# Performance work log

Measured on AMD Instinct MI355X. Metric: run time of the kernel, lower is better.

Reference implementation:

```python
import jax, jax.numpy as jnp
import numpy as np

D_STATE = 128   # Mamba2 default (the SS2D d_state=16 is never forwarded to Mamba2)
N_HEADS = 4     # d_ssm // headdim = d_model / (d_model//4)
D_CONV = 4
EPS = 1e-5


def silu(v):
    return v * jax.nn.sigmoid(v)


def setup_inputs() -> dict:
    key = jax.random.key(0)
    ks = jax.random.split(key, 12)
    d_model = 256
    d_inner = 2 * d_model            # expand=2
    d_ssm = d_model
    conv_dim = d_ssm + 2 * D_STATE   # 512
    d_in_proj = 2 * d_inner + 2 * D_STATE + N_HEADS  # 1284
    B, H, W = 8, 64, 64
    inp = {
        "x": jax.random.normal(ks[0], (B, d_model, H, W), jnp.float32),
        "in_proj_w": jax.random.normal(ks[1], (d_in_proj, d_model), jnp.float32) * 0.02,
        "conv_w": jax.random.normal(ks[2], (conv_dim, D_CONV), jnp.float32) * 0.2,
        "conv_b": jnp.zeros((conv_dim,), jnp.float32),
        "dt_bias": jax.random.normal(ks[3], (N_HEADS,), jnp.float32) * 0.1,
        "A_log": jnp.log(jax.random.uniform(ks[4], (N_HEADS,), jnp.float32, 1.0, 16.0)),
        "D": jax.random.normal(ks[5], (N_HEADS,), jnp.float32),
        "norm_w": jnp.ones((d_ssm,), jnp.float32),
        "out_proj_w": jax.random.normal(ks[6], (d_model, d_inner), jnp.float32) * 0.02,
        "se_w1": jax.random.normal(ks[7], (d_model // 4, d_model), jnp.float32) * 0.05,
        "se_b1": jnp.zeros((d_model // 4,), jnp.float32),
        "se_w2": jax.random.normal(ks[8], (d_model, d_model // 4), jnp.float32) * 0.05,
        "se_b2": jnp.zeros((d_model,), jnp.float32),
    }
    return inp


def _forward(x, in_proj_w, conv_w, conv_b, dt_bias, A_log, D, norm_w,
             out_proj_w, se_w1, se_b1, se_w2, se_b2):
    Bb, C, H, W = x.shape
    L = H * W
    d_model = C
    d_inner = 2 * d_model
    d_ssm = d_model
    d_mlp = d_inner - d_ssm
    headdim = d_ssm // N_HEADS
    conv_dim = d_ssm + 2 * D_STATE

    u = x.reshape(Bb, C, L).transpose(0, 2, 1)              # (b, l, c)
    zxbcdt = u @ in_proj_w.T                                 # (b, l, 1284)
    z0 = zxbcdt[..., :d_mlp]
    x0 = zxbcdt[..., d_mlp:2 * d_mlp]
    z = zxbcdt[..., 2 * d_mlp:2 * d_mlp + d_ssm]
    xBC = zxbcdt[..., 2 * d_mlp + d_ssm:2 * d_mlp + d_ssm + conv_dim]
    dt = zxbcdt[..., -N_HEADS:]

    dt = jax.nn.softplus(dt + dt_bias)                       # (b, l, h)

    # causal depthwise conv along l, kernel size D_CONV
    xpad = jnp.pad(xBC, ((0, 0), (D_CONV - 1, 0), (0, 0)))
    xconv = conv_b
    for k in range(D_CONV):
        xconv = xconv + xpad[:, k:k + L, :] * conv_w[:, k]
    xconv = silu(xconv)

    xs = xconv[..., :d_ssm]
    Bm = xconv[..., d_ssm:d_ssm + D_STATE]                   # (b, l, n) ngroups=1
    Cm = xconv[..., d_ssm + D_STATE:]                        # (b, l, n)
    xh = xs.reshape(Bb, L, N_HEADS, headdim)                 # (b, l, h, p)

    A = -jnp.exp(A_log)                                      # (h,)

    def step(hstate, inp):
        xt, dtt, Bt, Ct = inp  # (b,h,p), (b,h), (b,n), (b,n)
        dA = jnp.exp(dtt * A)                                # (b, h)
        hstate = hstate * dA[:, :, None, None] + \
            (dtt[:, :, None, None] * xt[..., None]) * Bt[:, None, None, :]
        y = jnp.einsum('bhpn,bn->bhp', hstate, Ct)
        return hstate, y

    h0 = jnp.zeros((Bb, N_HEADS, headdim, D_STATE), x.dtype)
    _, ys = jax.lax.scan(
        step, h0,
        (xh.transpose(1, 0, 2, 3), dt.transpose(1, 0, 2),
         Bm.transpose(1, 0, 2), Cm.transpose(1, 0, 2)))
    y = ys.transpose(1, 0, 2, 3)                             # (b, l, h, p)
    y = y + D[None, None, :, None] * xh                      # skip
    y = y.reshape(Bb, L, d_ssm)

    # gated RMSNorm (norm_before_gate=False): gate then normalize
    y = y * silu(z)
    y = y * jax.lax.rsqrt(jnp.mean(y * y, axis=-1, keepdims=True) + EPS) * norm_w

    y = jnp.concatenate([silu(z0) * x0, y], axis=-1)         # (b, l, d_inner)
    out = y @ out_proj_w.T                                   # (b, l, d_model)
    out = out.transpose(0, 2, 1).reshape(Bb, C, H, W)

    # SE-style spectral attention
    s = out.mean(axis=(2, 3))                                # (b, c)
    s = jax.nn.relu(s @ se_w1.T + se_b1)
    s = jax.nn.sigmoid(s @ se_w2.T + se_b2)
    return out * s[:, :, None, None]


def reference(x, in_proj_w, conv_w, conv_b, dt_bias, A_log, D, norm_w,
              out_proj_w, se_w1, se_b1, se_w2, se_b2):
    return _forward(x, in_proj_w, conv_w, conv_b, dt_bias, A_log, D, norm_w,
                    out_proj_w, se_w1, se_b1, se_w2, se_b2)
```

## Files before the change

### kernel.cpp

```cpp
#include <hip/hip_runtime.h>
#include <stdint.h>

typedef __attribute__((ext_vector_type(8))) short bf16x8;
typedef __attribute__((ext_vector_type(4))) float f32x4;

__device__ __forceinline__ float bf2f(unsigned short u) {
  unsigned int x = ((unsigned int)u) << 16;
  return __builtin_bit_cast(float, x);
}
__device__ __forceinline__ unsigned short f2bf(float f) {
  unsigned int x = __builtin_bit_cast(unsigned int, f);
  unsigned int r = x + 0x7FFFu + ((x >> 16) & 1u);
  return (unsigned short)(r >> 16);
}
__device__ __forceinline__ float silu(float v) { return v / (1.f + __expf(-v)); }
__device__ __forceinline__ f32x4 fz4() { f32x4 z; z[0]=0.f; z[1]=0.f; z[2]=0.f; z[3]=0.f; return z; }

#define LSEQ 4096
#define DMODEL 256
#define NIN 1284
#define NINP 1408

__global__ __launch_bounds__(256) void k_prep(const float* __restrict__ w_in,
                                              const float* __restrict__ w_out,
                                              unsigned short* __restrict__ wpad,
                                              unsigned short* __restrict__ woutbf,
                                              const float* __restrict__ x,
                                              unsigned short* __restrict__ ubf) {
  int bid = blockIdx.x;
  int tid = threadIdx.x;
  if (bid < 1920) {
    int idx = bid * 256 + tid;
    const int tot1 = NINP * DMODEL;
    if (idx < tot1) {
      int n = idx / DMODEL, k = idx % DMODEL;
      int src = (n < 512) ? ((n & 1) ? 256 + (n >> 1) : (n >> 1)) : n;
      float v = (src < NIN) ? w_in[src * DMODEL + k] : 0.f;
      wpad[idx] = f2bf(v);
    } else {
      int j = idx - tot1;
      woutbf[j] = f2bf(w_out[j]);
    }
    return;
  }
  __shared__ float t[64][65];
  int r = (bid - 1920) & 255;
  int b = (bid - 1920) >> 8;
  int lt = r >> 2, kt = r & 3;
  int l0 = lt * 64, k0 = kt * 64;
  int j = tid & 63, i0 = tid >> 6;
  for (int rr = 0; rr < 16; rr++) {
    int ki = i0 + rr * 4;
    t[ki][j] = x[(size_t)(b * DMODEL + k0 + ki) * LSEQ + l0 + j];
  }
  __syncthreads();
  for (int rr = 0; rr < 16; rr++) {
    int li = i0 + rr * 4;
    ubf[(size_t)(b * LSEQ + l0 + li) * DMODEL + k0 + j] = f2bf(t[j][li]);
  }
}

template <int KDIM, int LDA, int LDB, int EPI>
__global__ __launch_bounds__(256) void k_gemm(const unsigned short* __restrict__ A,
                                              const unsigned short* __restrict__ B,
                                              float* __restrict__ outF,
                                              unsigned short* __restrict__ outBF,
                                              unsigned short* __restrict__ outBF2,
                                              float* __restrict__ dtb, int tilesN) {
  __shared__ __align__(16) short lds[17408];
  short* As = lds;
  short* Bs = lds + 8192;
  int nwg = gridDim.x;
  int orig = blockIdx.x;
  int wgid = (nwg & 7) ? orig : ((orig & 7) * (nwg >> 3) + (orig >> 3));
  int tn = wgid % tilesN, tm = wgid / tilesN;
  int m0 = tm * 128, n0 = tn * 128;
  int tid = threadIdx.x;
  int w = tid >> 6, lane = tid & 63;
  int wr = w >> 1, wc = w & 1;
  f32x4 acc[4][4];
  for (int i = 0; i < 4; i++)
    for (int j = 0; j < 4; j++) acc[i][j] = fz4();

  for (int kt = 0; kt < KDIM / 64; kt++) {
    int k0 = kt * 64;
    for (int i = 0; i < 4; i++) {
      int rowblk = w * 32 + i * 8;
      int row = rowblk + (lane >> 3);
      int kc = ((lane & 7) ^ (row & 7)) * 8;
      const unsigned short* ga = A + (size_t)(m0 + row) * LDA + k0 + kc;
      __builtin_amdgcn_global_load_lds((const __attribute__((address_space(1))) unsigned int*)ga,
                                       (__attribute__((address_space(3))) unsigned int*)&As[rowblk * 64],
                                       16, 0, 0);
      const unsigned short* gb = B + (size_t)(n0 + row) * LDB + k0 + kc;
      __builtin_amdgcn_global_load_lds((const __attribute__((address_space(1))) unsigned int*)gb,
                                       (__attribute__((address_space(3))) unsigned int*)&Bs[rowblk * 64],
                                       16, 0, 0);
    }
    __syncthreads();
    for (int kk = 0; kk < 64; kk += 32) {
      int gq = (kk >> 3) + (lane >> 4);
      bf16x8 af[4], bfr[4];
      for (int mi = 0; mi < 4; mi++) {
        int rt = wr * 64 + mi * 16 + (lane & 15);
        af[mi] = *(const bf16x8*)((const char*)As + rt * 128 + ((gq ^ (rt & 7)) << 4));
      }
      for (int ni = 0; ni < 4; ni++) {
        int rs = wc * 64 + ni * 16 + (lane & 15);
        bfr[ni] = *(const bf16x8*)((const char*)Bs + rs * 128 + ((gq ^ (rs & 7)) << 4));
      }
      for (int mi = 0; mi < 4; mi++)
        for (int ni = 0; ni < 4; ni++)
          acc[mi][ni] = __builtin_amdgcn_mfma_f32_16x16x32_bf16(af[mi], bfr[ni], acc[mi][ni], 0, 0, 0);
    }
    __syncthreads();
  }

  int fq = lane >> 4, fr = lane & 15;
  if constexpr (EPI == 1) {
    float* Cf = (float*)lds;
    for (int ph = 0; ph < 2; ph++) {
      if (ph) __syncthreads();
      if (wc == ph) {
        for (int mi = 0; mi < 4; mi++)
          for (int ni = 0; ni < 4; ni++)
            for (int j = 0; j < 4; j++)
              Cf[(wr * 64 + mi * 16 + fq * 4 + j) * 68 + ni * 16 + fr] = acc[mi][ni][j];
      }
      __syncthreads();
      int rr = tid >> 4, cc = (tid & 15) * 4;
      for (int it = 0; it < 8; it++) {
        int r = it * 16 + rr;
        float4 v = *(const float4*)&Cf[r * 68 + cc];
        *(float4*)&outF[(size_t)(m0 + r) * 256 + n0 + ph * 64 + cc] = v;
      }
    }
  } else if constexpr (EPI == 2) {
    unsigned short* xbc = (unsigned short*)outF;
    if (n0 >= 1280) {
      if (wc == 0 && fr < 4) {
        for (int mi = 0; mi < 4; mi++)
          for (int j = 0; j < 4; j++) {
            int m = m0 + wr * 64 + mi * 16 + fq * 4 + j;
            dtb[m * 4 + fr] = acc[mi][0][j];
          }
      }
    } else if (n0 < 512) {
      short* Ct = lds;
      for (int mi = 0; mi < 4; mi++)
        for (int ni = 0; ni < 4; ni++)
          for (int j = 0; j < 4; j++) {
            float v = acc[mi][ni][j];
            float vp = __shfl_xor(v, 1, 64);
            if (!(fr & 1)) {
              float zc = silu(v) * vp;
              Ct[(wr * 64 + mi * 16 + fq * 4 + j) * 72 + wc * 32 + ni * 8 + (fr >> 1)] =
                  (short)f2bf(zc);
            }
          }
      __syncthreads();
      int r = tid >> 1, base = (tid & 1) * 32;
      for (int it = 0; it < 4; it++) {
        int cc = base + it * 8;
        uint4 v = *(const uint4*)&Ct[r * 72 + cc];
        *(uint4*)&outBF[(size_t)(m0 + r) * 512 + (n0 >> 1) + cc] = v;
      }
    } else {
      short* Ct = lds;
      for (int mi = 0; mi < 4; mi++)
        for (int ni = 0; ni < 4; ni++)
          for (int j = 0; j < 4; j++)
            Ct[(wr * 64 + mi * 16 + fq * 4 + j) * 136 + wc * 64 + ni * 16 + fr] =
                (short)f2bf(acc[mi][ni][j]);
      __syncthreads();
      int rr = tid >> 4, cc = (tid & 15) * 8;
      for (int it = 0; it < 8; it++) {
        int r = it * 16 + rr;
        uint4 v = *(const uint4*)&Ct[r * 136 + cc];
        if (n0 < 768) *(uint4*)&outBF2[(size_t)(m0 + r) * 256 + (n0 - 512) + cc] = v;
        else *(uint4*)&xbc[(size_t)(m0 + r) * 512 + (n0 - 768) + cc] = v;
      }
    }
  } else {
    bool dttile = (n0 >= 1280);
    if (dttile) {
      if (wc == 0 && fr < 4) {
        for (int mi = 0; mi < 4; mi++)
          for (int j = 0; j < 4; j++) {
            int m = m0 + wr * 64 + mi * 16 + fq * 4 + j;
            dtb[m * 4 + fr] = acc[mi][0][j];
          }
      }
    } else {
      short* Ct = lds;
      for (int mi = 0; mi < 4; mi++)
        for (int ni = 0; ni < 4; ni++)
          for (int j = 0; j < 4; j++)
            Ct[(wr * 64 + mi * 16 + fq * 4 + j) * 136 + wc * 64 + ni * 16 + fr] =
                (short)f2bf(acc[mi][ni][j]);
      __syncthreads();
      int rr = tid >> 4, cc = (tid & 15) * 8;
      for (int it = 0; it < 8; it++) {
        int r = it * 16 + rr;
        uint4 v = *(const uint4*)&Ct[r * 136 + cc];
        *(uint4*)&outBF[(size_t)(m0 + r) * 1280 + n0 + cc] = v;
      }
    }
  }
}

__global__ __launch_bounds__(256) void k_conv(const unsigned short* __restrict__ src, int stride,
                                              const float* __restrict__ conv_w,
                                              const float* __restrict__ conv_b,
                                              unsigned short* __restrict__ xs,
                                              unsigned short* __restrict__ bc,
                                              unsigned short* __restrict__ xsT,
                                              unsigned short* __restrict__ bT,
                                              const float* __restrict__ dtraw,
                                              const float* __restrict__ dt_bias,
                                              const float* __restrict__ A_log,
                                              float* __restrict__ dts,
                                              float* __restrict__ cums) {
  __shared__ __align__(16) unsigned short xt[35 * 512];
  int bid = blockIdx.x;
  int tid = threadIdx.x;
  if (bid >= 1024) {
    int w4 = tid >> 6, lane = tid & 63;
    int gc = (bid - 1024) * 4 + w4;
    int bh = gc >> 6, cc = gc & 63;
    int b2 = bh >> 2, h2 = bh & 3;
    int t = cc * 64 + lane;
    float v = dtraw[(size_t)(b2 * LSEQ + t) * 4 + h2] + dt_bias[h2];
    float dt = (v > 20.f) ? v : log1pf(__expf(v));
    float Ah = -__expf(A_log[h2]);
    float s = dt * Ah;
    for (int off = 1; off < 64; off <<= 1) {
      float o = __shfl_up(s, off, 64);
      if (lane >= off) s += o;
    }
    dts[bh * LSEQ + t] = dt;
    cums[bh * LSEQ + t] = s;
    return;
  }
  int b = bid >> 7;
  int t0 = (bid & 127) * 32;
  for (int id = tid; id < 35 * 64; id += 256) {
    int r = id >> 6, ch = id & 63;
    int t = t0 - 3 + r;
    float4 v;
    if (t < 0) v = make_float4(0.f, 0.f, 0.f, 0.f);
    else v = *(const float4*)&src[(size_t)(b * LSEQ + t) * stride + ch * 8];
    *(float4*)&xt[r * 512 + ch * 8] = v;
  }
  __syncthreads();
  int c0 = tid, c1 = tid + 256;
  float w0[4], w1[4];
  for (int k = 0; k < 4; k++) { w0[k] = conv_w[c0 * 4 + k]; w1[k] = conv_w[c1 * 4 + k]; }
  float bb0 = conv_b[c0], bb1 = conv_b[c1];
  unsigned short xa0[32], xa1[32];
#pragma unroll
  for (int tl = 0; tl < 32; tl++) {
    float a0 = bb0, a1 = bb1;
    for (int k = 0; k < 4; k++) {
      a0 += bf2f(xt[(tl + k) * 512 + c0]) * w0[k];
      a1 += bf2f(xt[(tl + k) * 512 + c1]) * w1[k];
    }
    a0 = silu(a0); a1 = silu(a1);
    unsigned short u0 = f2bf(a0), u1 = f2bf(a1);
    xa0[tl] = u0; xa1[tl] = u1;
    size_t row = (size_t)(b * LSEQ + t0 + tl);
    xs[row * 256 + c0] = u0;
    bc[row * 256 + (c1 - 256)] = u1;
  }
  if (xsT) {
    const uint4* p0 = (const uint4*)xa0;
    for (int k = 0; k < 4; k++)
      *(uint4*)&xsT[((size_t)(b * 256 + c0)) * LSEQ + t0 + k * 8] = p0[k];
    if (c1 < 384) {
      const uint4* p1 = (const uint4*)xa1;
      for (int k = 0; k < 4; k++)
        *(uint4*)&bT[((size_t)(b * 128 + (c1 - 256))) * LSEQ + t0 + k * 8] = p1[k];
    }
  }
}

__global__ __launch_bounds__(256) void k_scan(const unsigned short* __restrict__ xs,
                                              const unsigned short* __restrict__ bc,
                                              const float* __restrict__ dtb,
                                              const float* __restrict__ dt_bias,
                                              const float* __restrict__ A_log,
                                              const float* __restrict__ Dp,
                                              unsigned short* __restrict__ y) {
  __shared__ __align__(16) unsigned short bcl[32 * 256];
  __shared__ float xsl[32][4];
  __shared__ float dtl[32], dal[32];
  int bid = blockIdx.x;
  int b = bid >> 6;
  int h = (bid >> 4) & 3;
  int pg = bid & 15;
  int tid = threadIdx.x, w = tid >> 6, lane = tid & 63;
  int p = pg * 4 + w;
  float Ah = -expf(A_log[h]);
  float Dh = Dp[h];
  float bias = dt_bias[h];
  float h0 = 0.f, h1 = 0.f;
  for (int t0 = 0; t0 < LSEQ; t0 += 32) {
    for (int id = tid; id < 32 * 32; id += 256) {
      int r = id >> 5, ch = id & 31;
      *(float4*)&bcl[r * 256 + ch * 8] =
          *(const float4*)&bc[(size_t)(b * LSEQ + t0 + r) * 256 + ch * 8];
    }
    if (tid < 128) {
      int r = tid >> 2, pp = tid & 3;
      xsl[r][pp] = bf2f(xs[(size_t)(b * LSEQ + t0 + r) * 256 + h * 64 + pg * 4 + pp]);
    } else if (tid < 160) {
      int r = tid - 128;
      float v = dtb[(size_t)(b * LSEQ + t0 + r) * 4 + h] + bias;
      float dt = (v > 20.f) ? v : log1pf(expf(v));
      dtl[r] = dt;
      dal[r] = expf(dt * Ah);
    }
    __syncthreads();
    for (int tl = 0; tl < 32; tl++) {
      float dtv = dtl[tl], dav = dal[tl], xv = xsl[tl][w];
      float bn  = bf2f(bcl[tl * 256 + lane]);
      float bn2 = bf2f(bcl[tl * 256 + 64 + lane]);
      float cn  = bf2f(bcl[tl * 256 + 128 + lane]);
      float cn2 = bf2f(bcl[tl * 256 + 192 + lane]);
      float coef = dtv * xv;
      h0 = h0 * dav + coef * bn;
      h1 = h1 * dav + coef * bn2;
      float part = h0 * cn + h1 * cn2;
      for (int off = 32; off; off >>= 1) part += __shfl_xor(part, off, 64);
      if (lane == 0)
        y[(size_t)(b * LSEQ + t0 + tl) * 256 + h * 64 + p] = f2bf(part + Dh * xv);
    }
    __syncthreads();
  }
}

__global__ __launch_bounds__(256) void k_chunkA(const unsigned short* __restrict__ bc,
                                                const unsigned short* __restrict__ xsT,
                                                const unsigned short* __restrict__ bT,
                                                const float* __restrict__ dts,
                                                const float* __restrict__ cums,
                                                float* __restrict__ ST,
                                                unsigned short* __restrict__ yb) {
  __shared__ __align__(16) unsigned short Bsm[64 * 128];
  __shared__ __align__(16) unsigned short BTs[128 * 64];
  __shared__ __align__(16) unsigned short XT[64 * 64];
  __shared__ __align__(16) unsigned short Ms[64 * 72];
  __shared__ float dtl[64], cuml[64], scl[64];
  int bid = blockIdx.x;
  int bh = bid >> 6, c = bid & 63;
  int b = bh >> 2, h = bh & 3;
  int m0 = b * LSEQ + c * 64;
  int tid = threadIdx.x, w = tid >> 6, lane = tid & 63;

  if (tid < 64) {
    dtl[tid] = dts[bh * LSEQ + c * 64 + tid];
    cuml[tid] = cums[bh * LSEQ + c * 64 + tid];
  }
  __syncthreads();
  float cumQ = cuml[63];

  for (int it = 0; it < 4; it++) {
    int idx = it * 256 + tid, row = idx >> 4, g = idx & 15;
    uint4 v = *(const uint4*)&bc[(size_t)(m0 + row) * 256 + g * 8];
    *(uint4*)((char*)Bsm + row * 256 + ((g ^ (row & 7)) << 4)) = v;
  }
  for (int it = 0; it < 2; it++) {
    int idx = it * 256 + tid, row = idx >> 3, g = idx & 7;
    uint4 v = *(const uint4*)&xsT[((size_t)(b * 256 + h * 64 + row)) * LSEQ + c * 64 + g * 8];
    *(uint4*)((char*)XT + row * 128 + ((g ^ (row & 7)) << 4)) = v;
  }
  if (tid < 64) scl[tid] = dtl[tid] * __expf(cumQ - cuml[tid]);
  __syncthreads();
  for (int it = 0; it < 4; it++) {
    int idx = it * 256 + tid, row = idx >> 3, g = idx & 7;
    uint4 v = *(const uint4*)&bT[((size_t)(b * 128 + row)) * LSEQ + c * 64 + g * 8];
    const unsigned short* pv = (const unsigned short*)&v;
    uint4 o; unsigned short* po = (unsigned short*)&o;
#pragma unroll
    for (int e = 0; e < 8; e++) po[e] = f2bf(bf2f(pv[e]) * scl[g * 8 + e]);
    *(uint4*)((char*)BTs + row * 128 + ((g ^ (row & 7)) << 4)) = o;
  }

  int rt = w * 16 + (lane & 15);
  const unsigned short* arow = bc + (size_t)(m0 + rt) * 256 + 128;
  f32x4 acc1[4];
#pragma unroll
  for (int i = 0; i < 4; i++) acc1[i] = fz4();
#pragma unroll
  for (int ks = 0; ks < 4; ks++) {
    int g = ks * 4 + (lane >> 4);
    bf16x8 a = *(const bf16x8*)&arow[g * 8];
#pragma unroll
    for (int ni = 0; ni < 4; ni++) {
      int rs = ni * 16 + (lane & 15);
      bf16x8 bfr = *(const bf16x8*)((char*)Bsm + rs * 256 + ((g ^ (rs & 7)) << 4));
      acc1[ni] = __builtin_amdgcn_mfma_f32_16x16x32_bf16(a, bfr, acc1[ni], 0, 0, 0);
    }
  }
#pragma unroll
  for (int ni = 0; ni < 4; ni++)
#pragma unroll
    for (int j = 0; j < 4; j++) {
      int t = w * 16 + (lane >> 4) * 4 + j;
      int s = ni * 16 + (lane & 15);
      float v = 0.f;
      if (t >= s) v = acc1[ni][j] * __expf(cuml[t] - cuml[s]) * dtl[s];
      *(unsigned short*)((char*)Ms + t * 128 + (((s >> 3) ^ (t & 7)) << 4) + ((s & 7) << 1)) = f2bf(v);
    }
  __syncthreads();

  f32x4 acc2[4], acc3[8];
#pragma unroll
  for (int i = 0; i < 4; i++) acc2[i] = fz4();
#pragma unroll
  for (int i = 0; i < 8; i++) acc3[i] = fz4();
#pragma unroll
  for (int ks = 0; ks < 2; ks++) {
    int g = ks * 4 + (lane >> 4);
    bf16x8 xf[4];
#pragma unroll
    for (int ni = 0; ni < 4; ni++) {
      int rp = ni * 16 + (lane & 15);
      xf[ni] = *(const bf16x8*)((char*)XT + rp * 128 + ((g ^ (rp & 7)) << 4));
    }
    {
      bf16x8 a = *(const bf16x8*)((char*)Ms + rt * 128 + ((g ^ (rt & 7)) << 4));
#pragma unroll
      for (int ni = 0; ni < 4; ni++)
        acc2[ni] = __builtin_amdgcn_mfma_f32_16x16x32_bf16(a, xf[ni], acc2[ni], 0, 0, 0);
    }
    {
      bf16x8 a3 = xf[w];
#pragma unroll
      for (int ni = 0; ni < 8; ni++) {
        int rn = ni * 16 + (lane & 15);
        bf16x8 bfr = *(const bf16x8*)((char*)BTs + rn * 128 + ((g ^ (rn & 7)) << 4));
        acc3[ni] = __builtin_amdgcn_mfma_f32_16x16x32_bf16(a3, bfr, acc3[ni], 0, 0, 0);
      }
    }
  }
  __syncthreads();
#pragma unroll
  for (int ni = 0; ni < 4; ni++)
#pragma unroll
    for (int j = 0; j < 4; j++) {
      int t = w * 16 + (lane >> 4) * 4 + j;
      int p = ni * 16 + (lane & 15);
      Ms[t * 72 + p] = f2bf(acc2[ni][j]);
    }
  float* stp = ST + ((size_t)bid << 13);
#pragma unroll
  for (int ni = 0; ni < 8; ni++)
#pragma unroll
    for (int j = 0; j < 4; j++) {
      int p = w * 16 + (lane >> 4) * 4 + j;
      int n = ni * 16 + (lane & 15);
      stp[p * 128 + n] = acc3[ni][j];
    }
  __syncthreads();
  {
    int rr = tid >> 3, cc = (tid & 7) * 8;
    for (int it = 0; it < 2; it++) {
      int t = it * 32 + rr;
      uint4 v = *(const uint4*)&Ms[t * 72 + cc];
      *(uint4*)&yb[(size_t)(m0 + t) * 256 + h * 64 + cc] = v;
    }
  }
}

__global__ __launch_bounds__(256) void k_chunkB(const float* __restrict__ ST,
                                                const float* __restrict__ cums,
                                                unsigned short* __restrict__ HT) {
  int bid = blockIdx.x;
  int bh = bid >> 3, psl = bid & 7;
  int p = psl * 8 + (threadIdx.x >> 5);
  int n0 = (threadIdx.x & 31) * 4;
  float H[4] = {0.f, 0.f, 0.f, 0.f};
  for (int c = 0; c < 64; c++) {
    size_t base = (size_t)(bh * 64 + c);
    ushort4 hv;
    unsigned short* ha = (unsigned short*)&hv;
#pragma unroll
    for (int e = 0; e < 4; e++) ha[e] = f2bf(H[e]);
    *(ushort4*)&HT[(base * 64 + p) * 128 + n0] = hv;
    float4 s4 = *(const float4*)&ST[(base << 13) + p * 128 + n0];
    float dec = __expf(cums[bh * LSEQ + c * 64 + 63]);
    H[0] = H[0] * dec + s4.x;
    H[1] = H[1] * dec + s4.y;
    H[2] = H[2] * dec + s4.z;
    H[3] = H[3] * dec + s4.w;
  }
}

__global__ __launch_bounds__(256) void k_chunkC(const unsigned short* __restrict__ bc,
                                                const unsigned short* __restrict__ xs,
                                                const unsigned short* __restrict__ HT,
                                                const float* __restrict__ cums,
                                                const float* __restrict__ Dp,
                                                unsigned short* __restrict__ yb) {
  __shared__ __align__(16) unsigned short Hs[64 * 128];
  __shared__ __align__(16) unsigned short yst[64 * 72];
  int bid = blockIdx.x;
  int bh = bid >> 6, c = bid & 63;
  int b = bh >> 2, h = bh & 3;
  int m0 = b * LSEQ + c * 64;
  int tid = threadIdx.x, w = tid >> 6, lane = tid & 63;
  float Dh = Dp[h];
  for (int it = 0; it < 4; it++) {
    int idx = it * 256 + tid, row = idx >> 4, g = idx & 15;
    uint4 v = *(const uint4*)&HT[((size_t)(bh * 64 + c) * 64 + row) * 128 + g * 8];
    *(uint4*)((char*)Hs + row * 256 + ((g ^ (row & 7)) << 4)) = v;
  }
  float exq[4];
  {
    int tb = w * 16 + (lane >> 4) * 4;
#pragma unroll
    for (int j = 0; j < 4; j++) exq[j] = __expf(cums[bh * LSEQ + c * 64 + tb + j]);
  }
  __syncthreads();
  int rt = w * 16 + (lane & 15);
  const unsigned short* arow = bc + (size_t)(m0 + rt) * 256 + 128;
  f32x4 acc[4];
#pragma unroll
  for (int i = 0; i < 4; i++) acc[i] = fz4();
#pragma unroll
  for (int ks = 0; ks < 4; ks++) {
    int g = ks * 4 + (lane >> 4);
    bf16x8 a = *(const bf16x8*)&arow[g * 8];
#pragma unroll
    for (int ni = 0; ni < 4; ni++) {
      int rp = ni * 16 + (lane & 15);
      bf16x8 bfr = *(const bf16x8*)((char*)Hs + rp * 256 + ((g ^ (rp & 7)) << 4));
      acc[ni] = __builtin_amdgcn_mfma_f32_16x16x32_bf16(a, bfr, acc[ni], 0, 0, 0);
    }
  }
#pragma unroll
  for (int ni = 0; ni < 4; ni++)
#pragma unroll
    for (int j = 0; j < 4; j++) {
      int t = w * 16 + (lane >> 4) * 4 + j;
      int p = ni * 16 + (lane & 15);
      yst[t * 72 + p] = f2bf(acc[ni][j] * exq[j]);
    }
  __syncthreads();
  {
    int rr = tid >> 3, cc = (tid & 7) * 8;
    for (int it = 0; it < 2; it++) {
      int t = it * 32 + rr;
      size_t off = (size_t)(m0 + t) * 256 + h * 64 + cc;
      uint4 yo = *(const uint4*)&yb[off];
      uint4 xv = *(const uint4*)&xs[off];
      const unsigned short* pyo = (const unsigned short*)&yo;
      const unsigned short* pxv = (const unsigned short*)&xv;
      const unsigned short* pys = &yst[t * 72 + cc];
      uint4 vo;
      unsigned short* po = (unsigned short*)&vo;
#pragma unroll
      for (int e = 0; e < 8; e++)
        po[e] = f2bf(bf2f(pyo[e]) + bf2f(pys[e]) + Dh * bf2f(pxv[e]));
      *(uint4*)&yb[off] = vo;
    }
  }
}

template <int MODE>
__global__ __launch_bounds__(256) void k_ycat(const unsigned short* __restrict__ y,
                                              const unsigned short* __restrict__ zsrc,
                                              const float* __restrict__ norm_w,
                                              unsigned short* __restrict__ ocat) {
  int bid = blockIdx.x;
  int tid = threadIdx.x, w = tid >> 6, lane = tid & 63;
  size_t m = (size_t)bid * 4 + w;
  int j0 = lane * 4;
  ushort4 yv = *(const ushort4*)&y[m * 256 + j0];
  ushort4 zv;
  if constexpr (MODE == 0) zv = *(const ushort4*)&zsrc[m * 256 + j0];
  else zv = *(const ushort4*)&zsrc[m * 1280 + 512 + j0];
  unsigned short ya[4] = {yv.x, yv.y, yv.z, yv.w};
  unsigned short za[4] = {zv.x, zv.y, zv.z, zv.w};
  float g[4]; float ssum = 0.f;
  for (int i = 0; i < 4; i++) {
    float gg = bf2f(ya[i]) * silu(bf2f(za[i]));
    g[i] = gg; ssum += gg * gg;
  }
  for (int off = 32; off; off >>= 1) ssum += __shfl_xor(ssum, off, 64);
  float inv = rsqrtf(ssum * (1.f / 256.f) + 1e-5f);
  ushort4 o2;
  unsigned short* o2a = (unsigned short*)&o2;
  for (int i = 0; i < 4; i++) o2a[i] = f2bf(g[i] * norm_w[j0 + i] * inv);
  *(ushort4*)&ocat[m * 512 + 256 + j0] = o2;
  if constexpr (MODE == 1) {
    ushort4 p0 = *(const ushort4*)&zsrc[m * 1280 + 2 * j0];
    ushort4 p1 = *(const ushort4*)&zsrc[m * 1280 + 2 * j0 + 4];
    ushort4 o1;
    unsigned short* o1a = (unsigned short*)&o1;
    o1a[0] = f2bf(silu(bf2f(p0.x)) * bf2f(p0.y));
    o1a[1] = f2bf(silu(bf2f(p0.z)) * bf2f(p0.w));
    o1a[2] = f2bf(silu(bf2f(p1.x)) * bf2f(p1.y));
    o1a[3] = f2bf(silu(bf2f(p1.z)) * bf2f(p1.w));
    *(ushort4*)&ocat[m * 512 + j0] = o1;
  }
}

__global__ void k_zero(float* __restrict__ p) { p[blockIdx.x * 256 + threadIdx.x] = 0.f; }

__global__ __launch_bounds__(256) void k_semean(const float* __restrict__ res, float* __restrict__ smean) {
  int bid = blockIdx.x;
  int b = bid >> 5, ch = bid & 31;
  int c = threadIdx.x;
  float acc = 0.f;
  for (int r = 0; r < 128; r++)
    acc += res[(size_t)(b * LSEQ + ch * 128 + r) * 256 + c];
  atomicAdd(&smean[b * 256 + c], acc);
}

__global__ __launch_bounds__(512) void k_sefc(const float* __restrict__ smean,
                                              const float* __restrict__ w1, const float* __restrict__ b1,
                                              const float* __restrict__ w2, const float* __restrict__ b2,
                                              float* __restrict__ s2) {
  __shared__ float s1[512];
  int tid = threadIdx.x;
  int b = tid >> 6, j = tid & 63;
  float acc = b1[j];
  for (int k = 0; k < 256; k++) acc += smean[b * 256 + k] * (1.f / 4096.f) * w1[j * 256 + k];
  s1[b * 64 + j] = fmaxf(acc, 0.f);
  __syncthreads();
  for (int idx = tid; idx < 2048; idx += 512) {
    int bb = idx >> 8, c = idx & 255;
    float a2 = b2[c];
    for (int k = 0; k < 64; k++) a2 += s1[bb * 64 + k] * w2[c * 64 + k];
    s2[idx] = 1.f / (1.f + expf(-a2));
  }
}

__global__ __launch_bounds__(256) void k_final(const float* __restrict__ res,
                                               const float* __restrict__ s2,
                                               float* __restrict__ out) {
  __shared__ float t[64][65];
  int bid = blockIdx.x;
  int b = bid >> 8;
  int r = bid & 255;
  int ct = r >> 6, lt = r & 63;
  int c0 = ct * 64, l0 = lt * 64;
  int tid = threadIdx.x, j = tid & 63, i0 = tid >> 6;
  for (int rr = 0; rr < 16; rr++) {
    int i = i0 + rr * 4;
    t[i][j] = res[(size_t)(b * LSEQ + l0 + i) * 256 + c0 + j];
  }
  __syncthreads();
  for (int rr = 0; rr < 16; rr++) {
    int ci = i0 + rr * 4;
    float s = s2[b * 256 + c0 + ci];
    out[(size_t)(b * 256 + c0 + ci) * LSEQ + l0 + j] = t[j][ci] * s;
  }
}

extern "C" void kernel_launch(void* const* d_in, const int* in_sizes, int n_in,
                              void* d_out, int out_size, void* d_ws, size_t ws_size,
                              hipStream_t stream) {
  const float* x         = (const float*)d_in[0];
  const float* in_proj_w = (const float*)d_in[1];
  const float* conv_w    = (const float*)d_in[2];
  const float* conv_b    = (const float*)d_in[3];
  const float* dt_bias   = (const float*)d_in[4];
  const float* A_log     = (const float*)d_in[5];
  const float* Dp        = (const float*)d_in[6];
  const float* norm_w    = (const float*)d_in[7];
  const float* out_projw = (const float*)d_in[8];
  const float* se_w1     = (const float*)d_in[9];
  const float* se_b1     = (const float*)d_in[10];
  const float* se_w2     = (const float*)d_in[11];
  const float* se_b2     = (const float*)d_in[12];
  float* out = (float*)d_out;
  char* ws = (char*)d_ws;

  const size_t NEED_CHUNKED = 220676096;

  if (ws_size >= NEED_CHUNKED) {
    float*          ST    = (float*)(ws + 0);
    unsigned short* ubf   = (unsigned short*)(ws + 0);
    unsigned short* xbc   = (unsigned short*)(ws + 16777216);
    float*          res   = (float*)(ws + 0);
    unsigned short* zcat  = (unsigned short*)(ws + 67108864);
    unsigned short* zbuf  = (unsigned short*)(ws + 100663296);
    unsigned short* xsb   = (unsigned short*)(ws + 117440512);
    unsigned short* bcb   = (unsigned short*)(ws + 134217728);
    unsigned short* HT    = (unsigned short*)(ws + 150994944);
    unsigned short* xsT   = (unsigned short*)(ws + 150994944);
    unsigned short* bT    = (unsigned short*)(ws + 167772160);
    unsigned short* ybuf  = (unsigned short*)(ws + 184549376);
    unsigned short* wpad  = (unsigned short*)(ws + 201326592);
    unsigned short* woutb = (unsigned short*)(ws + 202047488);
    float*          dtraw = (float*)(ws + 202309632);
    float*          dts   = (float*)(ws + 202833920);
    float*          cums  = (float*)(ws + 203358208);
    float*          smean = (float*)(ws + 203882496);
    float*          s2    = (float*)(ws + 203890688);

    k_prep<<<3968, 256, 0, stream>>>(in_proj_w, out_projw, wpad, woutb, x, ubf);
    k_gemm<256, 256, 256, 2><<<256 * 11, 256, 0, stream>>>(ubf, wpad, (float*)xbc, zcat, zbuf, dtraw, 11);
    k_conv<<<1536, 256, 0, stream>>>(xbc, 512, conv_w, conv_b, xsb, bcb, xsT, bT,
                                     dtraw, dt_bias, A_log, dts, cums);
    k_chunkA<<<2048, 256, 0, stream>>>(bcb, xsT, bT, dts, cums, ST, ybuf);
    k_chunkB<<<256, 256, 0, stream>>>(ST, cums, HT);
    k_chunkC<<<2048, 256, 0, stream>>>(bcb, xsb, HT, cums, Dp, ybuf);
    k_ycat<0><<<8192, 256, 0, stream>>>(ybuf, zbuf, norm_w, zcat);
    k_gemm<512, 512, 512, 1><<<256 * 2, 256, 0, stream>>>(zcat, woutb, res, nullptr, nullptr, nullptr, 2);
    k_zero<<<8, 256, 0, stream>>>(smean);
    k_semean<<<256, 256, 0, stream>>>(res, smean);
    k_sefc<<<1, 512, 0, stream>>>(smean, se_w1, se_b1, se_w2, se_b2, s2);
    k_final<<<2048, 256, 0, stream>>>(res, s2, out);
  } else {
    unsigned short* ubf   = (unsigned short*)(ws + 0);
    unsigned short* xsb   = (unsigned short*)(ws + 16777216);
    float*          res   = (float*)(ws + 0);
    unsigned short* bcb   = (unsigned short*)(ws + 33554432);
    unsigned short* zx    = (unsigned short*)(ws + 50331648);
    float*          dtb   = (float*)(ws + 134217728);
    unsigned short* ybuf  = (unsigned short*)(ws + 134742016);
    unsigned short* ycat  = (unsigned short*)(ws + 151519232);
    unsigned short* wpad  = (unsigned short*)(ws + 185073664);
    unsigned short* woutb = (unsigned short*)(ws + 185794560);
    float*          smean = (float*)(ws + 186056704);
    float*          s2    = (float*)(ws + 186064896);

    k_prep<<<3968, 256, 0, stream>>>(in_proj_w, out_projw, wpad, woutb, x, ubf);
    k_gemm<256, 256, 256, 0><<<256 * 11, 256, 0, stream>>>(ubf, wpad, nullptr, zx, nullptr, dtb, 11);
    k_conv<<<1024, 256, 0, stream>>>(zx + 768, 1280, conv_w, conv_b, xsb, bcb, nullptr, nullptr,
                                     nullptr, nullptr, nullptr, nullptr, nullptr);
    k_scan<<<512, 256, 0, stream>>>(xsb, bcb, dtb, dt_bias, A_log, Dp, ybuf);
    k_ycat<1><<<8192, 256, 0, stream>>>(ybuf, zx, norm_w, ycat);
    k_gemm<512, 512, 512, 1><<<256 * 2, 256, 0, stream>>>(ycat, woutb, res, nullptr, nullptr, nullptr, 2);
    k_zero<<<8, 256, 0, stream>>>(smean);
    k_semean<<<256, 256, 0, stream>>>(res, smean);
    k_sefc<<<1, 512, 0, stream>>>(smean, se_w1, se_b1, se_w2, se_b2, s2);
    k_final<<<2048, 256, 0, stream>>>(res, s2, out);
  }
}
```

Baseline: 226.3 us.

## Store out-proj result transposed in bf16 and chunk states in bf16

```diff
diff --git a/kernel.cpp b/kernel.cpp
--- a/kernel.cpp
+++ b/kernel.cpp
@@ -118,22 +118,24 @@
 
   int fq = lane >> 4, fr = lane & 15;
   if constexpr (EPI == 1) {
-    float* Cf = (float*)lds;
-    for (int ph = 0; ph < 2; ph++) {
-      if (ph) __syncthreads();
-      if (wc == ph) {
-        for (int mi = 0; mi < 4; mi++)
-          for (int ni = 0; ni < 4; ni++)
-            for (int j = 0; j < 4; j++)
-              Cf[(wr * 64 + mi * 16 + fq * 4 + j) * 68 + ni * 16 + fr] = acc[mi][ni][j];
-      }
-      __syncthreads();
-      int rr = tid >> 4, cc = (tid & 15) * 4;
-      for (int it = 0; it < 8; it++) {
-        int r = it * 16 + rr;
-        float4 v = *(const float4*)&Cf[r * 68 + cc];
-        *(float4*)&outF[(size_t)(m0 + r) * 256 + n0 + ph * 64 + cc] = v;
-      }
+    short* Ct = lds;
+    for (int mi = 0; mi < 4; mi++)
+      for (int ni = 0; ni < 4; ni++)
+        for (int j = 0; j < 4; j++) {
+          int r = wr * 64 + mi * 16 + fq * 4 + j;
+          int cch = wc * 64 + ni * 16 + fr;
+          Ct[cch * 136 + r] = (short)f2bf(acc[mi][ni][j]);
+        }
+    __syncthreads();
+    int b = m0 >> 12, l0 = m0 & 4095;
+    for (int it = 0; it < 4; it++) {
+      int row = it * 32 + (tid >> 3);
+      int cc = (tid & 7) * 16;
+      uint4 v0 = *(const uint4*)&Ct[row * 136 + cc];
+      uint4 v1 = *(const uint4*)&Ct[row * 136 + cc + 8];
+      unsigned short* dst = outBF + ((size_t)(b * 256 + n0 + row)) * 4096 + l0 + cc;
+      *(uint4*)dst = v0;
+      *(uint4*)&dst[8] = v1;
     }
   } else if constexpr (EPI == 2) {
     unsigned short* xbc = (unsigned short*)outF;
@@ -344,12 +346,13 @@
                                                 const unsigned short* __restrict__ bT,
                                                 const float* __restrict__ dts,
                                                 const float* __restrict__ cums,
-                                                float* __restrict__ ST,
+                                                unsigned short* __restrict__ ST,
                                                 unsigned short* __restrict__ yb) {
-  __shared__ __align__(16) unsigned short Bsm[64 * 128];
-  __shared__ __align__(16) unsigned short BTs[128 * 64];
-  __shared__ __align__(16) unsigned short XT[64 * 64];
-  __shared__ __align__(16) unsigned short Ms[64 * 72];
+  __shared__ __align__(16) unsigned short sh[25088];
+  unsigned short* Bsm = sh;
+  unsigned short* BTs = sh + 8192;
+  unsigned short* XT  = sh + 16384;
+  unsigned short* Ms  = sh + 20480;
   __shared__ float dtl[64], cuml[64], scl[64];
   int bid = blockIdx.x;
   int bh = bid >> 6, c = bid & 63;
@@ -445,6 +448,7 @@
     }
   }
   __syncthreads();
+  unsigned short* STst = sh;
 #pragma unroll
   for (int ni = 0; ni < 4; ni++)
 #pragma unroll
@@ -453,14 +457,13 @@
       int p = ni * 16 + (lane & 15);
       Ms[t * 72 + p] = f2bf(acc2[ni][j]);
     }
-  float* stp = ST + ((size_t)bid << 13);
 #pragma unroll
   for (int ni = 0; ni < 8; ni++)
 #pragma unroll
     for (int j = 0; j < 4; j++) {
       int p = w * 16 + (lane >> 4) * 4 + j;
       int n = ni * 16 + (lane & 15);
-      stp[p * 128 + n] = acc3[ni][j];
+      STst[p * 136 + n] = f2bf(acc3[ni][j]);
     }
   __syncthreads();
   {
@@ -471,9 +474,17 @@
       *(uint4*)&yb[(size_t)(m0 + t) * 256 + h * 64 + cc] = v;
     }
   }
-}
-
-__global__ __launch_bounds__(256) void k_chunkB(const float* __restrict__ ST,
+  {
+    unsigned short* stp = ST + ((size_t)bid << 13);
+    int rr = tid >> 2, cc = (tid & 3) * 32;
+    for (int q = 0; q < 4; q++) {
+      uint4 v = *(const uint4*)&STst[rr * 136 + cc + q * 8];
+      *(uint4*)&stp[rr * 128 + cc + q * 8] = v;
+    }
+  }
+}
+
+__global__ __launch_bounds__(256) void k_chunkB(const unsigned short* __restrict__ ST,
                                                 const float* __restrict__ cums,
                                                 unsigned short* __restrict__ HT) {
   int bid = blockIdx.x;
@@ -488,12 +499,12 @@
 #pragma unroll
     for (int e = 0; e < 4; e++) ha[e] = f2bf(H[e]);
     *(ushort4*)&HT[(base * 64 + p) * 128 + n0] = hv;
-    float4 s4 = *(const float4*)&ST[(base << 13) + p * 128 + n0];
+    ushort4 s4 = *(const ushort4*)&ST[(base << 13) + p * 128 + n0];
     float dec = __expf(cums[bh * LSEQ + c * 64 + 63]);
-    H[0] = H[0] * dec + s4.x;
-    H[1] = H[1] * dec + s4.y;
-    H[2] = H[2] * dec + s4.z;
-    H[3] = H[3] * dec + s4.w;
+    H[0] = H[0] * dec + bf2f(s4.x);
+    H[1] = H[1] * dec + bf2f(s4.y);
+    H[2] = H[2] * dec + bf2f(s4.z);
+    H[3] = H[3] * dec + bf2f(s4.w);
   }
 }
 
@@ -607,16 +618,23 @@
   }
 }
 
-__global__ void k_zero(float* __restrict__ p) { p[blockIdx.x * 256 + threadIdx.x] = 0.f; }
-
-__global__ __launch_bounds__(256) void k_semean(const float* __restrict__ res, float* __restrict__ smean) {
-  int bid = blockIdx.x;
-  int b = bid >> 5, ch = bid & 31;
-  int c = threadIdx.x;
+__global__ __launch_bounds__(256) void k_semean(const unsigned short* __restrict__ rest,
+                                                float* __restrict__ smean) {
+  __shared__ float wsum[4];
+  int row = blockIdx.x;
+  int tid = threadIdx.x, w = tid >> 6, lane = tid & 63;
+  const unsigned short* p = rest + (size_t)row * 4096;
   float acc = 0.f;
-  for (int r = 0; r < 128; r++)
-    acc += res[(size_t)(b * LSEQ + ch * 128 + r) * 256 + c];
-  atomicAdd(&smean[b * 256 + c], acc);
+  for (int it = 0; it < 2; it++) {
+    uint4 v = *(const uint4*)&p[(it * 256 + tid) * 8];
+    const unsigned short* pv = (const unsigned short*)&v;
+#pragma unroll
+    for (int e = 0; e < 8; e++) acc += bf2f(pv[e]);
+  }
+  for (int off = 32; off; off >>= 1) acc += __shfl_xor(acc, off, 64);
+  if (lane == 0) wsum[w] = acc;
+  __syncthreads();
+  if (tid == 0) smean[row] = wsum[0] + wsum[1] + wsum[2] + wsum[3];
 }
 
 __global__ __launch_bounds__(512) void k_sefc(const float* __restrict__ smean,
@@ -638,25 +656,25 @@
   }
 }
 
-__global__ __launch_bounds__(256) void k_final(const float* __restrict__ res,
+__global__ __launch_bounds__(256) void k_final(const unsigned short* __restrict__ rest,
                                                const float* __restrict__ s2,
                                                float* __restrict__ out) {
-  __shared__ float t[64][65];
-  int bid = blockIdx.x;
-  int b = bid >> 8;
-  int r = bid & 255;
-  int ct = r >> 6, lt = r & 63;
-  int c0 = ct * 64, l0 = lt * 64;
-  int tid = threadIdx.x, j = tid & 63, i0 = tid >> 6;
-  for (int rr = 0; rr < 16; rr++) {
-    int i = i0 + rr * 4;
-    t[i][j] = res[(size_t)(b * LSEQ + l0 + i) * 256 + c0 + j];
-  }
-  __syncthreads();
-  for (int rr = 0; rr < 16; rr++) {
-    int ci = i0 + rr * 4;
-    float s = s2[b * 256 + c0 + ci];
-    out[(size_t)(b * 256 + c0 + ci) * LSEQ + l0 + j] = t[j][ci] * s;
+  int row = blockIdx.x;
+  float s = s2[row];
+  int tid = threadIdx.x;
+  const unsigned short* p = rest + (size_t)row * 4096;
+  float* o = out + (size_t)row * 4096;
+  for (int it = 0; it < 2; it++) {
+    int base = (it * 256 + tid) * 8;
+    uint4 v = *(const uint4*)&p[base];
+    const unsigned short* pv = (const unsigned short*)&v;
+    float4 f0, f1;
+    f0.x = bf2f(pv[0]) * s; f0.y = bf2f(pv[1]) * s;
+    f0.z = bf2f(pv[2]) * s; f0.w = bf2f(pv[3]) * s;
+    f1.x = bf2f(pv[4]) * s; f1.y = bf2f(pv[5]) * s;
+    f1.z = bf2f(pv[6]) * s; f1.w = bf2f(pv[7]) * s;
+    *(float4*)&o[base] = f0;
+    *(float4*)&o[base + 4] = f1;
   }
 }
 
@@ -682,10 +700,10 @@
   const size_t NEED_CHUNKED = 220676096;
 
   if (ws_size >= NEED_CHUNKED) {
-    float*          ST    = (float*)(ws + 0);
+    unsigned short* ST16  = (unsigned short*)(ws + 0);
     unsigned short* ubf   = (unsigned short*)(ws + 0);
     unsigned short* xbc   = (unsigned short*)(ws + 16777216);
-    float*          res   = (float*)(ws + 0);
+    unsigned short* res16 = (unsigned short*)(ws + 0);
     unsigned short* zcat  = (unsigned short*)(ws + 67108864);
     unsigned short* zbuf  = (unsigned short*)(ws + 100663296);
     unsigned short* xsb   = (unsigned short*)(ws + 117440512);
@@ -706,19 +724,18 @@
     k_gemm<256, 256, 256, 2><<<256 * 11, 256, 0, stream>>>(ubf, wpad, (float*)xbc, zcat, zbuf, dtraw, 11);
     k_conv<<<1536, 256, 0, stream>>>(xbc, 512, conv_w, conv_b, xsb, bcb, xsT, bT,
                                      dtraw, dt_bias, A_log, dts, cums);
-    k_chunkA<<<2048, 256, 0, stream>>>(bcb, xsT, bT, dts, cums, ST, ybuf);
-    k_chunkB<<<256, 256, 0, stream>>>(ST, cums, HT);
+    k_chunkA<<<2048, 256, 0, stream>>>(bcb, xsT, bT, dts, cums, ST16, ybuf);
+    k_chunkB<<<256, 256, 0, stream>>>(ST16, cums, HT);
     k_chunkC<<<2048, 256, 0, stream>>>(bcb, xsb, HT, cums, Dp, ybuf);
     k_ycat<0><<<8192, 256, 0, stream>>>(ybuf, zbuf, norm_w, zcat);
-    k_gemm<512, 512, 512, 1><<<256 * 2, 256, 0, stream>>>(zcat, woutb, res, nullptr, nullptr, nullptr, 2);
-    k_zero<<<8, 256, 0, stream>>>(smean);
-    k_semean<<<256, 256, 0, stream>>>(res, smean);
+    k_gemm<512, 512, 512, 1><<<256 * 2, 256, 0, stream>>>(zcat, woutb, nullptr, res16, nullptr, nullptr, 2);
+    k_semean<<<2048, 256, 0, stream>>>(res16, smean);
     k_sefc<<<1, 512, 0, stream>>>(smean, se_w1, se_b1, se_w2, se_b2, s2);
-    k_final<<<2048, 256, 0, stream>>>(res, s2, out);
+    k_final<<<2048, 256, 0, stream>>>(res16, s2, out);
   } else {
     unsigned short* ubf   = (unsigned short*)(ws + 0);
+    unsigned short* res16 = (unsigned short*)(ws + 0);
     unsigned short* xsb   = (unsigned short*)(ws + 16777216);
-    float*          res   = (float*)(ws + 0);
     unsigned short* bcb   = (unsigned short*)(ws + 33554432);
     unsigned short* zx    = (unsigned short*)(ws + 50331648);
     float*          dtb   = (float*)(ws + 134217728);
@@ -735,10 +752,9 @@
                                      nullptr, nullptr, nullptr, nullptr, nullptr);
     k_scan<<<512, 256, 0, stream>>>(xsb, bcb, dtb, dt_bias, A_log, Dp, ybuf);
     k_ycat<1><<<8192, 256, 0, stream>>>(ybuf, zx, norm_w, ycat);
-    k_gemm<512, 512, 512, 1><<<256 * 2, 256, 0, stream>>>(ycat, woutb, res, nullptr, nullptr, nullptr, 2);
-    k_zero<<<8, 256, 0, stream>>>(smean);
-    k_semean<<<256, 256, 0, stream>>>(res, smean);
+    k_gemm<512, 512, 512, 1><<<256 * 2, 256, 0, stream>>>(ycat, woutb, nullptr, res16, nullptr, nullptr, 2);
+    k_semean<<<2048, 256, 0, stream>>>(res16, smean);
     k_sefc<<<1, 512, 0, stream>>>(smean, se_w1, se_b1, se_w2, se_b2, s2);
-    k_final<<<2048, 256, 0, stream>>>(res, s2, out);
-  }
-}
+    k_final<<<2048, 256, 0, stream>>>(res16, s2, out);
+  }
+}
```

New measurement: 221.0 us. 1.02x faster.
